# Performance work log

Hardware: AMD Instinct MI355X
Metric: run time of the kernel (lower is better)

## Reference

```python
import jax, jax.numpy as jnp
import numpy as np

DIM = 1024
HEADS = 16
HIDDEN = 4 * DIM

def _gelu_erf(x):
    # GELU via erf, matching the torch module exactly
    return x * 0.5 * (1.0 + jax.lax.erf(x / jnp.sqrt(2.0).astype(x.dtype)))

def setup_inputs() -> dict:
    key = jax.random.key(0)
    ks = jax.random.split(key, 12)
    s = 0.02
    x = jax.random.normal(ks[0], (2, 2048, DIM), dtype=jnp.float32)
    # MHSA params
    ln1_g = jnp.ones((DIM,), jnp.float32)
    ln1_b = jnp.zeros((DIM,), jnp.float32)
    w_qkv = jax.random.normal(ks[1], (DIM, 3 * DIM), jnp.float32) * s  # no bias
    w_proj = jax.random.normal(ks[2], (DIM, DIM), jnp.float32) * s
    b_proj = jnp.zeros((DIM,), jnp.float32)
    # ResMLP params
    ln2_g = jnp.ones((DIM,), jnp.float32)
    ln2_b = jnp.zeros((DIM,), jnp.float32)
    w1 = jax.random.normal(ks[3], (DIM, HIDDEN), jnp.float32) * s
    b1 = jnp.zeros((HIDDEN,), jnp.float32)
    w2 = jax.random.normal(ks[4], (HIDDEN, DIM), jnp.float32) * s
    b2 = jnp.zeros((DIM,), jnp.float32)
    return {"x": x, "ln1_g": ln1_g, "ln1_b": ln1_b, "w_qkv": w_qkv,
            "w_proj": w_proj, "b_proj": b_proj, "ln2_g": ln2_g, "ln2_b": ln2_b,
            "w1": w1, "b1": b1, "w2": w2, "b2": b2}

def _layernorm(x, g, b, eps=1e-5):
    mu = jnp.mean(x, axis=-1, keepdims=True)
    var = jnp.mean(jnp.square(x - mu), axis=-1, keepdims=True)
    return (x - mu) * jax.lax.rsqrt(var + eps) * g + b

def reference(x, ln1_g, ln1_b, w_qkv, w_proj, b_proj, ln2_g, ln2_b, w1, b1, w2, b2):
    B, N, C = x.shape
    H = HEADS
    hd = C // H
    scale = hd ** -0.5
    # --- MHSA (dropout is identity in eval) ---
    h = _layernorm(x, ln1_g, ln1_b)
    qkv = (h @ w_qkv).reshape(B, N, 3, H, hd)
    q = jnp.transpose(qkv[:, :, 0], (0, 2, 1, 3))  # [B,H,N,hd]
    k = jnp.transpose(qkv[:, :, 1], (0, 2, 1, 3))
    v = jnp.transpose(qkv[:, :, 2], (0, 2, 1, 3))
    attn = jax.nn.softmax(jnp.einsum('bhnd,bhmd->bhnm', q, k) * scale, axis=-1)
    out = jnp.einsum('bhnm,bhmd->bhnd', attn, v)
    out = jnp.transpose(out, (0, 2, 1, 3)).reshape(B, N, C)
    x = x + out @ w_proj + b_proj
    # --- ResMLP ---
    h = _layernorm(x, ln2_g, ln2_b)
    h = _gelu_erf(h @ w1 + b1)
    x = x + h @ w2 + b2
    return x
```

## Files before the change

kernel.cpp:

```cpp
#include <hip/hip_runtime.h>
#include <stdint.h>


#define DIMC 1024
#define HIDN 4096
#define SEQ  2048
#define TOK  4096

typedef __bf16 bf16x8 __attribute__((ext_vector_type(8)));
typedef float  f32x4  __attribute__((ext_vector_type(4)));
typedef unsigned short ushort8 __attribute__((ext_vector_type(8)));

__device__ inline unsigned short f2bf(float f) {
  union { float f; unsigned u; } v; v.f = f;
  unsigned u = v.u;
  return (unsigned short)((u + 0x7fffu + ((u >> 16) & 1u)) >> 16);
}

__device__ inline unsigned cvt_pk_bf16(float a, float b) {
  unsigned r;
  asm("v_cvt_pk_bf16_f32 %0, %1, %2" : "=v"(r) : "v"(a), "v"(b));
  return r;
}

#if __has_builtin(__builtin_amdgcn_exp2f)
__device__ inline float fast_exp2(float x) { return __builtin_amdgcn_exp2f(x); }
#else
__device__ inline float fast_exp2(float x) { return exp2f(x); }
#endif

__device__ inline f32x4 mfma_bf16(bf16x8 a, bf16x8 b, f32x4 c) {
  return __builtin_amdgcn_mfma_f32_16x16x32_bf16(a, b, c, 0, 0, 0);
}

typedef const __attribute__((address_space(1))) unsigned int* as1_u32p;
typedef __attribute__((address_space(3))) unsigned int* as3_u32p;
__device__ inline void gload_lds16(const unsigned short* g, unsigned short* l) {
  __builtin_amdgcn_global_load_lds((as1_u32p)(const void*)g, (as3_u32p)(void*)l,
                                   16, 0, 0);
}

__global__ __launch_bounds__(256)
void transpose_cast4(const float* __restrict__ wa, unsigned short* __restrict__ ta,
                     const float* __restrict__ wb, unsigned short* __restrict__ tb,
                     const float* __restrict__ wc, unsigned short* __restrict__ tc,
                     const float* __restrict__ wd, unsigned short* __restrict__ td) {
  __shared__ float tile[32][33];
  const int bid = blockIdx.x;
  const float* w; unsigned short* wt; int K, N, bx, by;
  if (bid < 3072)      { w = wa; wt = ta; K = 1024; N = 3072; bx = bid % 96;  by = bid / 96; }
  else if (bid < 4096) { int i = bid - 3072; w = wb; wt = tb; K = 1024; N = 1024; bx = i % 32;  by = i / 32; }
  else if (bid < 8192) { int i = bid - 4096; w = wc; wt = tc; K = 1024; N = 4096; bx = i % 128; by = i / 128; }
  else                 { int i = bid - 8192; w = wd; wt = td; K = 4096; N = 1024; bx = i % 32;  by = i / 32; }
  const int k0 = by * 32;
  const int n0 = bx * 32;
  const int tx = threadIdx.x & 31;
  const int ty = threadIdx.x >> 5;
#pragma unroll
  for (int i = 0; i < 4; i++)
    tile[ty + i * 8][tx] = w[(size_t)(k0 + ty + i * 8) * N + n0 + tx];
  __syncthreads();
#pragma unroll
  for (int i = 0; i < 4; i++)
    wt[(size_t)(n0 + ty + i * 8) * K + k0 + tx] = f2bf(tile[tx][ty + i * 8]);
}

__global__ __launch_bounds__(256)
void ln_kernel(const float* __restrict__ x, const float* __restrict__ g,
               const float* __restrict__ b, unsigned short* __restrict__ out) {
  const int row = blockIdx.x;
  const int tid = threadIdx.x;
  const float4* xr = (const float4*)&x[(size_t)row * DIMC];
  float4 v = xr[tid];
  float s  = v.x + v.y + v.z + v.w;
  float sq = v.x * v.x + v.y * v.y + v.z * v.z + v.w * v.w;
#pragma unroll
  for (int off = 32; off > 0; off >>= 1) {
    s  += __shfl_xor(s, off, 64);
    sq += __shfl_xor(sq, off, 64);
  }
  __shared__ float red[8];
  if ((tid & 63) == 0) { red[tid >> 6] = s; red[4 + (tid >> 6)] = sq; }
  __syncthreads();
  s  = red[0] + red[1] + red[2] + red[3];
  sq = red[4] + red[5] + red[6] + red[7];
  const float mu  = s * (1.0f / DIMC);
  const float var = sq * (1.0f / DIMC) - mu * mu;
  const float rs  = rsqrtf(var + 1e-5f);
  const int c = tid * 4;
  float vv[4] = {v.x, v.y, v.z, v.w};
#pragma unroll
  for (int j = 0; j < 4; j++)
    out[(size_t)row * DIMC + c + j] = f2bf((vv[j] - mu) * rs * g[c + j] + b[c + j]);
}

template <int EPI, int TN>
__global__ __launch_bounds__(256, (TN == 64) ? 4 : 3)
void gemm_bt(const unsigned short* __restrict__ A,
             const unsigned short* __restrict__ Bt,
             float* __restrict__ Cf, unsigned short* __restrict__ Cb,
             const float* __restrict__ bias, const float* __restrict__ res,
             int M, int N, int K,
             unsigned short* __restrict__ qd,
             unsigned short* __restrict__ kTd,
             unsigned short* __restrict__ vTd) {
  constexpr int NU = TN / 32;
  constexpr int BP = TN / 32;
  __shared__ unsigned short As[128 * 64];
  __shared__ unsigned short Bs[TN * 64];
  const int gx  = N / TN;
  const int bid = blockIdx.x;
  const int xcd = bid & 7;
  const int lin = bid >> 3;
  const int bx  = lin % gx;
  const int by  = (xcd << 2) + lin / gx;
  const int tid  = threadIdx.x;
  const int lane = tid & 63;
  const int wave = tid >> 6;
  const int m0 = by * 128;
  const int n0 = bx * TN;
  const int wm = (wave >> 1) * 64;
  const int wn = (wave & 1) * (TN / 2);
  const int lm = lane & 15;
  const int lg = lane >> 4;
  const int r8 = tid >> 3;
  const int c8 = tid & 7;
  const int csrc = ((c8 ^ (r8 & 7)) * 8);

  const unsigned short* gA = &A [(size_t)(m0 + r8) * K + csrc];
  const unsigned short* gB = &Bt[(size_t)(n0 + r8) * K + csrc];

  f32x4 acc[4][NU];
#pragma unroll
  for (int t = 0; t < 4; t++)
#pragma unroll
    for (int u = 0; u < NU; u++) acc[t][u] = {0.f, 0.f, 0.f, 0.f};

  const int x0 = (lg ^ (lm & 7)) * 8;
  const int x1 = ((4 + lg) ^ (lm & 7)) * 8;

  for (int k0 = 0; k0 < K; k0 += 64) {
    __syncthreads();
#pragma unroll
    for (int p = 0; p < 4; p++)
      gload_lds16(gA + (size_t)p * 32 * K + k0, &As[p * 2048 + wave * 512]);
#pragma unroll
    for (int p = 0; p < BP; p++)
      gload_lds16(gB + (size_t)p * 32 * K + k0, &Bs[p * 2048 + wave * 512]);
    __syncthreads();
#pragma unroll
    for (int sub = 0; sub < 2; sub++) {
      const int xo = sub ? x1 : x0;
      bf16x8 af[4], bfr[NU];
#pragma unroll
      for (int t = 0; t < 4; t++)  af[t]  = *(const bf16x8*)&As[(wm + t * 16 + lm) * 64 + xo];
#pragma unroll
      for (int u = 0; u < NU; u++) bfr[u] = *(const bf16x8*)&Bs[(wn + u * 16 + lm) * 64 + xo];
#pragma unroll
      for (int t = 0; t < 4; t++)
#pragma unroll
        for (int u = 0; u < NU; u++)
          acc[t][u] = mfma_bf16(af[t], bfr[u], acc[t][u]);
    }
  }

#pragma unroll
  for (int t = 0; t < 4; t++) {
    const int row = m0 + wm + t * 16 + lg * 4;
#pragma unroll
    for (int u = 0; u < NU; u++) {
      const int col = n0 + wn + u * 16 + lm;
#pragma unroll
      for (int r = 0; r < 4; r++) {
        float v = acc[t][u][r];
        size_t idx = (size_t)(row + r) * N + col;
        if (EPI == 0) {
          const int rr = row + r;
          const int bb = rr >> 11, key = rr & (SEQ - 1);
          if (col < 1024) {
            qd[(size_t)rr * 1024 + col] = f2bf(v * 0.18033688011112042f);
          } else if (col < 2048) {
            const int d = col - 1024, h = d >> 6, dd = d & 63;
            kTd[(((size_t)(bb * 16 + h)) * SEQ + key) * 64 + dd] = f2bf(v);
          } else {
            const int d = col - 2048, h = d >> 6, dd = d & 63;
            vTd[(((size_t)(bb * 16 + h)) * 64 + dd) * SEQ + key] = f2bf(v);
          }
        } else if (EPI == 1) {
          Cf[idx] = v + bias[col] + res[idx];
        } else {
          float xg = v + bias[col];
          Cb[idx] = f2bf(0.5f * xg * (1.0f + erff(xg * 0.70710678118654752f)));
        }
      }
    }
  }
}

__global__ __launch_bounds__(128, 2)
void attn_kernel(const unsigned short* __restrict__ qbuf,
                 const unsigned short* __restrict__ kT,
                 const unsigned short* __restrict__ vT,
                 unsigned short* __restrict__ out) {
  const int bid = blockIdx.x;
  const int xcd = bid & 7;
  const int lin = bid >> 3;
  const int bh  = (xcd << 2) + (lin >> 4);
  const int qt  = lin & 15;
  const int b  = bh >> 4;
  const int h  = bh & 15;
  const int tid  = threadIdx.x;
  const int lane = tid & 63;
  const int wave = tid >> 6;
  const int lm = lane & 15;
  const int lg = lane >> 4;

  __shared__ unsigned short Ks[64 * 64];
  __shared__ unsigned short Vs[64 * 64];
  __shared__ unsigned short Ps[2][64 * 64];

  const int qrow_base = b * SEQ + qt * 128 + wave * 64;
  bf16x8 qb[4][2];
#pragma unroll
  for (int s = 0; s < 4; s++)
#pragma unroll
    for (int c = 0; c < 2; c++)
      qb[s][c] = *(const bf16x8*)&qbuf[(size_t)(qrow_base + s * 16 + lm) * 1024 +
                                       h * 64 + c * 32 + lg * 8];

  f32x4 o[4][4];
#pragma unroll
  for (int dt = 0; dt < 4; dt++)
#pragma unroll
    for (int s = 0; s < 4; s++) o[dt][s] = {0.f, 0.f, 0.f, 0.f};
  float li[4] = {0.f, 0.f, 0.f, 0.f};

  const unsigned short* kbp = &kT[(size_t)bh * SEQ * 64];
  const unsigned short* vbp = &vT[(size_t)bh * 64 * SEQ];
  const int srow = tid >> 3;
  const int slog = ((tid & 7) ^ (srow & 7)) * 8;
  const int xk0 = ((lg)     ^ (lm & 7)) * 8;
  const int xk1 = ((4 + lg) ^ (lm & 7)) * 8;

  for (int kt = 0; kt < SEQ / 64; kt++) {
    __syncthreads();
#pragma unroll
    for (int p = 0; p < 4; p++) {
      gload_lds16(&kbp[(size_t)kt * 4096 + (p * 16 + srow) * 64 + slog],
                  &Ks[p * 1024 + wave * 512]);
      gload_lds16(&vbp[(size_t)(p * 16 + srow) * SEQ + kt * 64 + slog],
                  &Vs[p * 1024 + wave * 512]);
    }
    __syncthreads();

#pragma unroll
    for (int u = 0; u < 4; u++) {
      bf16x8 ka0 = *(const bf16x8*)&Ks[(u * 16 + lm) * 64 + xk0];
      bf16x8 ka1 = *(const bf16x8*)&Ks[(u * 16 + lm) * 64 + xk1];
      f32x4 st[4];
#pragma unroll
      for (int s = 0; s < 4; s++) {
        f32x4 z = {0.f, 0.f, 0.f, 0.f};
        z = mfma_bf16(ka0, qb[s][0], z);
        z = mfma_bf16(ka1, qb[s][1], z);
        st[s] = z;
      }
#pragma unroll
      for (int s = 0; s < 4; s++) {
        float p0 = fast_exp2(st[s][0] - 8.0f);
        float p1 = fast_exp2(st[s][1] - 8.0f);
        float p2 = fast_exp2(st[s][2] - 8.0f);
        float p3 = fast_exp2(st[s][3] - 8.0f);
        li[s] += (p0 + p1) + (p2 + p3);
        uint2 pk;
        pk.x = cvt_pk_bf16(p0, p1);
        pk.y = cvt_pk_bf16(p2, p3);
        const int phys = (u * 2 + (lg >> 1)) ^ (lm & 7);
        *(uint2*)&Ps[wave][(s * 16 + lm) * 64 + phys * 8 + (lg & 1) * 4] = pk;
      }
    }

#pragma unroll
    for (int kc = 0; kc < 2; kc++) {
      const int xo = kc ? xk1 : xk0;
      bf16x8 pb[4];
#pragma unroll
      for (int s = 0; s < 4; s++)
        pb[s] = *(const bf16x8*)&Ps[wave][(s * 16 + lm) * 64 + xo];
#pragma unroll
      for (int dt = 0; dt < 4; dt++) {
        bf16x8 va = *(const bf16x8*)&Vs[(dt * 16 + lm) * 64 + xo];
#pragma unroll
        for (int s = 0; s < 4; s++)
          o[dt][s] = mfma_bf16(va, pb[s], o[dt][s]);
      }
    }
  }

#pragma unroll
  for (int s = 0; s < 4; s++) {
    float l = li[s];
    l += __shfl_xor(l, 16, 64);
    l += __shfl_xor(l, 32, 64);
    const float inv = 1.0f / l;
#pragma unroll
    for (int dt = 0; dt < 4; dt++) {
      uint2 ok;
      ok.x = cvt_pk_bf16(o[dt][s][0] * inv, o[dt][s][1] * inv);
      ok.y = cvt_pk_bf16(o[dt][s][2] * inv, o[dt][s][3] * inv);
      *(uint2*)&out[(size_t)(qrow_base + s * 16 + lm) * DIMC + h * 64 +
                    dt * 16 + lg * 4] = ok;
    }
  }
}

extern "C" void kernel_launch(void* const* d_in, const int* in_sizes, int n_in,
                              void* d_out, int out_size, void* d_ws, size_t ws_size,
                              hipStream_t stream) {
  const float* x      = (const float*)d_in[0];
  const float* ln1_g  = (const float*)d_in[1];
  const float* ln1_b  = (const float*)d_in[2];
  const float* w_qkv  = (const float*)d_in[3];
  const float* w_proj = (const float*)d_in[4];
  const float* b_proj = (const float*)d_in[5];
  const float* ln2_g  = (const float*)d_in[6];
  const float* ln2_b  = (const float*)d_in[7];
  const float* w1     = (const float*)d_in[8];
  const float* b1     = (const float*)d_in[9];
  const float* w2     = (const float*)d_in[10];
  const float* b2     = (const float*)d_in[11];
  float* out = (float*)d_out;

  char* ws = (char*)d_ws;
  size_t off = 0;
  auto alloc = [&](size_t bytes) { void* p = ws + off; off += (bytes + 255) & ~(size_t)255; return p; };
  unsigned short* wqkvT = (unsigned short*)alloc((size_t)3072 * 1024 * 2);
  unsigned short* wprjT = (unsigned short*)alloc((size_t)1024 * 1024 * 2);
  unsigned short* w1T   = (unsigned short*)alloc((size_t)4096 * 1024 * 2);
  unsigned short* w2T   = (unsigned short*)alloc((size_t)1024 * 4096 * 2);
  unsigned short* hb    = (unsigned short*)alloc((size_t)TOK * 1024 * 2);
  unsigned short* qbuf  = (unsigned short*)alloc((size_t)TOK * 1024 * 2);
  unsigned short* attnb = (unsigned short*)alloc((size_t)TOK * 1024 * 2);
  float*          x1    = (float*)         alloc((size_t)TOK * 1024 * 4);
  unsigned short* hidb  = (unsigned short*)alloc((size_t)TOK * 4096 * 2);
  unsigned short* kT = hidb;
  unsigned short* vT = hidb + (size_t)32 * SEQ * 64;

  transpose_cast4<<<12288, 256, 0, stream>>>(w_qkv, wqkvT, w_proj, wprjT,
                                             w1, w1T, w2, w2T);
  ln_kernel<<<TOK, 256, 0, stream>>>(x, ln1_g, ln1_b, hb);
  gemm_bt<0, 128><<<768, 256, 0, stream>>>(
      hb, wqkvT, nullptr, nullptr, nullptr, nullptr, TOK, 3072, 1024,
      qbuf, kT, vT);
  attn_kernel<<<512, 128, 0, stream>>>(qbuf, kT, vT, attnb);
  gemm_bt<1, 64><<<512, 256, 0, stream>>>(
      attnb, wprjT, x1, nullptr, b_proj, x, TOK, 1024, 1024,
      nullptr, nullptr, nullptr);
  ln_kernel<<<TOK, 256, 0, stream>>>(x1, ln2_g, ln2_b, hb);
  gemm_bt<2, 128><<<1024, 256, 0, stream>>>(
      hb, w1T, nullptr, hidb, b1, nullptr, TOK, 4096, 1024,
      nullptr, nullptr, nullptr);
  gemm_bt<1, 64><<<512, 256, 0, stream>>>(
      hidb, w2T, out, nullptr, b2, x1, TOK, 1024, 4096,
      nullptr, nullptr, nullptr);
}
```

Before: 374.1 us.

## Split attention keys across wave pairs and add separate V transpose kernel

The attention kernel now runs 256 threads, with two wave pairs each covering half of the key sequence for the same 128 queries. The partial outputs and row sums are combined through shared memory before normalisation, which doubles the waves working on each block. The QKV GEMM epilogue now writes V row-major, avoiding strided scattered stores, and a new kernel transposes V through an LDS tile. This adds a kernel launch, an extra round trip of V through memory, and a shared-memory reduction at the end of attention.

Measured after the change: 333.5 us. 10.9% less time.

```diff
diff --git a/kernel.cpp b/kernel.cpp
--- a/kernel.cpp
+++ b/kernel.cpp
@@ -103,7 +103,7 @@
              int M, int N, int K,
              unsigned short* __restrict__ qd,
              unsigned short* __restrict__ kTd,
-             unsigned short* __restrict__ vTd) {
+             unsigned short* __restrict__ vd) {
   constexpr int NU = TN / 32;
   constexpr int BP = TN / 32;
   __shared__ unsigned short As[128 * 64];
@@ -183,8 +183,7 @@
             const int d = col - 1024, h = d >> 6, dd = d & 63;
             kTd[(((size_t)(bb * 16 + h)) * SEQ + key) * 64 + dd] = f2bf(v);
           } else {
-            const int d = col - 2048, h = d >> 6, dd = d & 63;
-            vTd[(((size_t)(bb * 16 + h)) * 64 + dd) * SEQ + key] = f2bf(v);
+            vd[(size_t)rr * 1024 + (col - 2048)] = f2bf(v);
           }
         } else if (EPI == 1) {
           Cf[idx] = v + bias[col] + res[idx];
@@ -197,7 +196,35 @@
   }
 }
 
-__global__ __launch_bounds__(128, 2)
+__global__ __launch_bounds__(256)
+void v_transpose(const unsigned short* __restrict__ vd,
+                 unsigned short* __restrict__ vT) {
+  const int kt = blockIdx.x;
+  const int bh = blockIdx.y;
+  const int b = bh >> 4, h = bh & 15;
+  const int tid = threadIdx.x;
+  __shared__ unsigned short tile[64 * 72];
+  const int tok = tid >> 2;
+  const int ch  = tid & 3;
+  const size_t srow = (size_t)(b * SEQ + kt * 64 + tok) * 1024 + h * 64;
+  ushort8 va = *(const ushort8*)&vd[srow + ch * 8];
+  ushort8 vb = *(const ushort8*)&vd[srow + 32 + ch * 8];
+  *(ushort8*)&tile[tok * 72 + ch * 8] = va;
+  *(ushort8*)&tile[tok * 72 + 32 + ch * 8] = vb;
+  __syncthreads();
+  const int d = tid >> 2;
+  ushort8 o0, o1;
+#pragma unroll
+  for (int j = 0; j < 8; j++) {
+    o0[j] = tile[(ch * 8 + j) * 72 + d];
+    o1[j] = tile[((ch + 4) * 8 + j) * 72 + d];
+  }
+  const size_t vdst = ((size_t)bh * 64 + d) * SEQ + kt * 64;
+  *(ushort8*)&vT[vdst + ch * 8] = o0;
+  *(ushort8*)&vT[vdst + 32 + ch * 8] = o1;
+}
+
+__global__ __launch_bounds__(256, 2)
 void attn_kernel(const unsigned short* __restrict__ qbuf,
                  const unsigned short* __restrict__ kT,
                  const unsigned short* __restrict__ vT,
@@ -212,14 +239,17 @@
   const int tid  = threadIdx.x;
   const int lane = tid & 63;
   const int wave = tid >> 6;
+  const int ks   = wave >> 1;
+  const int qh   = wave & 1;
   const int lm = lane & 15;
   const int lg = lane >> 4;
 
-  __shared__ unsigned short Ks[64 * 64];
-  __shared__ unsigned short Vs[64 * 64];
-  __shared__ unsigned short Ps[2][64 * 64];
-
-  const int qrow_base = b * SEQ + qt * 128 + wave * 64;
+  __shared__ f32x4 shbuf[4096];
+  unsigned short* Ks = (unsigned short*)shbuf;
+  unsigned short* Vs = (unsigned short*)shbuf + 8192;
+  unsigned short* Ps = (unsigned short*)shbuf + 16384;
+
+  const int qrow_base = b * SEQ + qt * 128 + qh * 64;
   bf16x8 qb[4][2];
 #pragma unroll
   for (int s = 0; s < 4; s++)
@@ -237,26 +267,33 @@
 
   const unsigned short* kbp = &kT[(size_t)bh * SEQ * 64];
   const unsigned short* vbp = &vT[(size_t)bh * 64 * SEQ];
-  const int srow = tid >> 3;
-  const int slog = ((tid & 7) ^ (srow & 7)) * 8;
+  const int ts   = tid & 127;
+  const int srow = ts >> 3;
+  const int slog = ((ts & 7) ^ (srow & 7)) * 8;
+  const int koff = ks * 1024;
   const int xk0 = ((lg)     ^ (lm & 7)) * 8;
   const int xk1 = ((4 + lg) ^ (lm & 7)) * 8;
-
-  for (int kt = 0; kt < SEQ / 64; kt++) {
+  unsigned short* ksb = Ks + ks * 4096;
+  unsigned short* vsb = Vs + ks * 4096;
+  unsigned short* psb = Ps + wave * 4096;
+  unsigned short* kdst = ksb + ((ts >> 6) * 512);
+  unsigned short* vdst = vsb + ((ts >> 6) * 512);
+
+  for (int kt = 0; kt < 16; kt++) {
     __syncthreads();
 #pragma unroll
     for (int p = 0; p < 4; p++) {
-      gload_lds16(&kbp[(size_t)kt * 4096 + (p * 16 + srow) * 64 + slog],
-                  &Ks[p * 1024 + wave * 512]);
-      gload_lds16(&vbp[(size_t)(p * 16 + srow) * SEQ + kt * 64 + slog],
-                  &Vs[p * 1024 + wave * 512]);
+      gload_lds16(&kbp[(size_t)(koff + kt * 64 + p * 16 + srow) * 64 + slog],
+                  kdst + p * 1024);
+      gload_lds16(&vbp[(size_t)(p * 16 + srow) * SEQ + koff + kt * 64 + slog],
+                  vdst + p * 1024);
     }
     __syncthreads();
 
 #pragma unroll
     for (int u = 0; u < 4; u++) {
-      bf16x8 ka0 = *(const bf16x8*)&Ks[(u * 16 + lm) * 64 + xk0];
-      bf16x8 ka1 = *(const bf16x8*)&Ks[(u * 16 + lm) * 64 + xk1];
+      bf16x8 ka0 = *(const bf16x8*)&ksb[(u * 16 + lm) * 64 + xk0];
+      bf16x8 ka1 = *(const bf16x8*)&ksb[(u * 16 + lm) * 64 + xk1];
       f32x4 st[4];
 #pragma unroll
       for (int s = 0; s < 4; s++) {
@@ -276,7 +313,7 @@
         pk.x = cvt_pk_bf16(p0, p1);
         pk.y = cvt_pk_bf16(p2, p3);
         const int phys = (u * 2 + (lg >> 1)) ^ (lm & 7);
-        *(uint2*)&Ps[wave][(s * 16 + lm) * 64 + phys * 8 + (lg & 1) * 4] = pk;
+        *(uint2*)&psb[(s * 16 + lm) * 64 + phys * 8 + (lg & 1) * 4] = pk;
       }
     }
 
@@ -286,10 +323,10 @@
       bf16x8 pb[4];
 #pragma unroll
       for (int s = 0; s < 4; s++)
-        pb[s] = *(const bf16x8*)&Ps[wave][(s * 16 + lm) * 64 + xo];
+        pb[s] = *(const bf16x8*)&psb[(s * 16 + lm) * 64 + xo];
 #pragma unroll
       for (int dt = 0; dt < 4; dt++) {
-        bf16x8 va = *(const bf16x8*)&Vs[(dt * 16 + lm) * 64 + xo];
+        bf16x8 va = *(const bf16x8*)&vsb[(dt * 16 + lm) * 64 + xo];
 #pragma unroll
         for (int s = 0; s < 4; s++)
           o[dt][s] = mfma_bf16(va, pb[s], o[dt][s]);
@@ -297,19 +334,39 @@
     }
   }
 
-#pragma unroll
-  for (int s = 0; s < 4; s++) {
-    float l = li[s];
-    l += __shfl_xor(l, 16, 64);
-    l += __shfl_xor(l, 32, 64);
-    const float inv = 1.0f / l;
-#pragma unroll
-    for (int dt = 0; dt < 4; dt++) {
-      uint2 ok;
-      ok.x = cvt_pk_bf16(o[dt][s][0] * inv, o[dt][s][1] * inv);
-      ok.y = cvt_pk_bf16(o[dt][s][2] * inv, o[dt][s][3] * inv);
-      *(uint2*)&out[(size_t)(qrow_base + s * 16 + lm) * DIMC + h * 64 +
-                    dt * 16 + lg * 4] = ok;
+  __syncthreads();
+  f32x4* ob = shbuf + qh * 1088;
+  float*  lb = (float*)(ob + 1024);
+  if (ks == 1) {
+#pragma unroll
+    for (int dt = 0; dt < 4; dt++)
+#pragma unroll
+      for (int s = 0; s < 4; s++)
+        ob[(dt * 4 + s) * 64 + lane] = o[dt][s];
+#pragma unroll
+    for (int s = 0; s < 4; s++) lb[s * 64 + lane] = li[s];
+  }
+  __syncthreads();
+  if (ks == 0) {
+#pragma unroll
+    for (int dt = 0; dt < 4; dt++)
+#pragma unroll
+      for (int s = 0; s < 4; s++)
+        o[dt][s] += ob[(dt * 4 + s) * 64 + lane];
+#pragma unroll
+    for (int s = 0; s < 4; s++) {
+      float l = li[s] + lb[s * 64 + lane];
+      l += __shfl_xor(l, 16, 64);
+      l += __shfl_xor(l, 32, 64);
+      const float inv = 1.0f / l;
+#pragma unroll
+      for (int dt = 0; dt < 4; dt++) {
+        uint2 ok;
+        ok.x = cvt_pk_bf16(o[dt][s][0] * inv, o[dt][s][1] * inv);
+        ok.y = cvt_pk_bf16(o[dt][s][2] * inv, o[dt][s][3] * inv);
+        *(uint2*)&out[(size_t)(qrow_base + s * 16 + lm) * DIMC + h * 64 +
+                      dt * 16 + lg * 4] = ok;
+      }
     }
   }
 }
@@ -340,6 +397,7 @@
   unsigned short* w2T   = (unsigned short*)alloc((size_t)1024 * 4096 * 2);
   unsigned short* hb    = (unsigned short*)alloc((size_t)TOK * 1024 * 2);
   unsigned short* qbuf  = (unsigned short*)alloc((size_t)TOK * 1024 * 2);
+  unsigned short* vdb   = (unsigned short*)alloc((size_t)TOK * 1024 * 2);
   unsigned short* attnb = (unsigned short*)alloc((size_t)TOK * 1024 * 2);
   float*          x1    = (float*)         alloc((size_t)TOK * 1024 * 4);
   unsigned short* hidb  = (unsigned short*)alloc((size_t)TOK * 4096 * 2);
@@ -351,8 +409,9 @@
   ln_kernel<<<TOK, 256, 0, stream>>>(x, ln1_g, ln1_b, hb);
   gemm_bt<0, 128><<<768, 256, 0, stream>>>(
       hb, wqkvT, nullptr, nullptr, nullptr, nullptr, TOK, 3072, 1024,
-      qbuf, kT, vT);
-  attn_kernel<<<512, 128, 0, stream>>>(qbuf, kT, vT, attnb);
+      qbuf, kT, vdb);
+  v_transpose<<<dim3(SEQ / 64, 32), 256, 0, stream>>>(vdb, vT);
+  attn_kernel<<<512, 256, 0, stream>>>(qbuf, kT, vT, attnb);
   gemm_bt<1, 64><<<512, 256, 0, stream>>>(
       attnb, wprjT, x1, nullptr, b_proj, x, TOK, 1024, 1024,
       nullptr, nullptr, nullptr);
```
